# Optimization experiments

Measured on AMD Instinct MI355X. Metric: run time of the kernel, lower is better.

The kernel has to match this reference:

```python
import jax, jax.numpy as jnp
import numpy as np

N = 100000   # nodes
D = 128      # feature dim
E = 1600000  # edges (avg degree 16)
BN_EPS = 1e-5


def setup_inputs() -> dict:
    key = jax.random.key(0)
    ks = jax.random.split(key, 8)
    x = jax.random.normal(ks[0], (N, D), dtype=jnp.float32)
    edge_index = jax.random.randint(ks[1], (2, E), 0, N, dtype=jnp.int64)
    W = jax.random.normal(ks[2], (D, D), dtype=jnp.float32) * 0.05   # GCNConv linear weight
    b = jax.random.normal(ks[3], (D,), dtype=jnp.float32) * 0.05     # GCNConv bias
    gamma = jax.random.uniform(ks[4], (D,), dtype=jnp.float32) + 0.5 # BN weight
    beta = jax.random.normal(ks[5], (D,), dtype=jnp.float32) * 0.1   # BN bias
    running_mean = jax.random.normal(ks[6], (D,), dtype=jnp.float32) * 0.1
    running_var = jax.random.uniform(ks[7], (D,), dtype=jnp.float32) + 0.5
    return {"x": x, "edge_index": edge_index, "W": W, "b": b,
            "gamma": gamma, "beta": beta,
            "running_mean": running_mean, "running_var": running_var}


def reference(x, edge_index, W, b, gamma, beta, running_mean, running_var):
    # --- GCNConv (default: add self-loops, symmetric normalization) ---
    h = x @ W                                        # [N, D]
    loops = jnp.arange(N, dtype=edge_index.dtype)
    src = jnp.concatenate([edge_index[0], loops])    # [E+N]
    dst = jnp.concatenate([edge_index[1], loops])    # [E+N]
    deg = jax.ops.segment_sum(jnp.ones_like(dst, dtype=h.dtype), dst, num_segments=N)
    dinv = jax.lax.rsqrt(jnp.maximum(deg, 1.0))      # deg >= 1 due to self-loops
    norm = dinv[src] * dinv[dst]                     # [E+N]
    agg = jax.ops.segment_sum(h[src] * norm[:, None], dst, num_segments=N)  # [N, D]
    agg = agg + b
    # --- BatchNorm1d (inference: running stats) ---
    bn = (agg - running_mean) * jax.lax.rsqrt(running_var + BN_EPS) * gamma + beta
    # --- ReLU + residual (dropout is identity in eval) ---
    return jax.nn.relu(bn) + x
```

## Files before the change

kernel.cpp:

```cpp
#include <hip/hip_runtime.h>

#define D 128
#define BN_EPS 1e-5f
#define NBUCK 512
#define BSHIFT 8
#define BNODES 256

using short8 = __attribute__((ext_vector_type(8))) short;
using floatx4 = __attribute__((ext_vector_type(4))) float;

__device__ inline unsigned short f2bf(float f) {
    unsigned u = __float_as_uint(f);
    u += 0x7fff + ((u >> 16) & 1);
    return (unsigned short)(u >> 16);
}
__device__ inline float bf2f(unsigned short s) {
    return __uint_as_float(((unsigned)s) << 16);
}

__global__ void wt_kernel(const float* __restrict__ W, const float* __restrict__ b,
                          const float* __restrict__ gamma, const float* __restrict__ beta,
                          const float* __restrict__ mean, const float* __restrict__ var,
                          unsigned short* __restrict__ Wt, float* __restrict__ scv,
                          float* __restrict__ pov) {
    int t = blockIdx.x * blockDim.x + threadIdx.x;
    int k = t >> 7, n = t & 127;
    Wt[(size_t)n * D + k] = f2bf(W[t]);
    if (t < D) {
        float sc = gamma[t] * rsqrtf(var[t] + BN_EPS);
        scv[t] = sc;
        pov[t] = (b[t] - mean[t]) * sc + beta[t];
    }
}

__global__ __launch_bounds__(512) void pAwt_kernel(
    const int* __restrict__ dst, int* __restrict__ bucketTot, int E,
    const float* __restrict__ W, const float* __restrict__ b,
    const float* __restrict__ gamma, const float* __restrict__ beta,
    const float* __restrict__ mean, const float* __restrict__ var,
    unsigned short* __restrict__ Wt, float* __restrict__ scv,
    float* __restrict__ pov) {
    __shared__ int lh[NBUCK];
    int tid = threadIdx.x;
    lh[tid] = 0;
    __syncthreads();
    for (int i = blockIdx.x * 512 + tid; i < E; i += gridDim.x * 512)
        atomicAdd(&lh[dst[i] >> BSHIFT], 1);
    if (blockIdx.x < 16) {
        int t = blockIdx.x * 512 + tid;
#pragma unroll
        for (int h = 0; h < 2; ++h) {
            int tt = t + h * 8192;
            Wt[(size_t)(tt & 127) * D + (tt >> 7)] = f2bf(W[tt]);
        }
        if (blockIdx.x == 0 && tid < D) {
            float sc = gamma[tid] * rsqrtf(var[tid] + BN_EPS);
            scv[tid] = sc;
            pov[tid] = (b[tid] - mean[tid]) * sc + beta[tid];
        }
    }
    __syncthreads();
    if (lh[tid]) atomicAdd(&bucketTot[tid], lh[tid]);
}

__global__ __launch_bounds__(512) void pB_kernel(const int* __restrict__ src,
                                                 const int* __restrict__ dst,
                                                 const int* __restrict__ bucketTot,
                                                 int* __restrict__ resCnt,
                                                 int2* __restrict__ pairs, int E) {
    __shared__ int sb[NBUCK];
    __shared__ int lh[NBUCK];
    __shared__ int lcur[NBUCK];
    int tid = threadIdx.x;
    sb[tid] = bucketTot[tid];
    lh[tid] = 0;
    __syncthreads();
    for (int d = 1; d < NBUCK; d <<= 1) {
        int v = (tid >= d) ? sb[tid - d] : 0;
        __syncthreads();
        sb[tid] += v;
        __syncthreads();
    }
    int chunk = (E + gridDim.x - 1) / gridDim.x;
    int base = blockIdx.x * chunk;
    int lim = min(chunk, E - base);
    if (lim <= 0) return;
    for (int i = tid; i < lim; i += 512) atomicAdd(&lh[dst[base + i] >> BSHIFT], 1);
    __syncthreads();
    int c = lh[tid];
    lcur[tid] = c ? (sb[tid] - bucketTot[tid]) + atomicAdd(&resCnt[tid], c) : 0;
    __syncthreads();
    for (int i = tid; i < lim; i += 512) {
        int s = src[base + i], d2 = dst[base + i];
        int pos = atomicAdd(&lcur[d2 >> BSHIFT], 1);
        pairs[pos] = make_int2(s, d2);
    }
}

__global__ __launch_bounds__(512) void sortxs_kernel(
    const int2* __restrict__ pairs, const int* __restrict__ bucketTot,
    const float* __restrict__ x, int* __restrict__ deg, int* __restrict__ offs,
    int* __restrict__ colidx, float* __restrict__ dinv,
    unsigned short* __restrict__ xs, int N, int E) {
    __shared__ int sb[NBUCK];
    __shared__ int lh[BNODES];
    __shared__ int lcur[BNODES];
    __shared__ float sdv[BNODES];
    int tid = threadIdx.x;
    int b = blockIdx.x;
    sb[tid] = bucketTot[tid];
    __syncthreads();
    for (int d = 1; d < NBUCK; d <<= 1) {
        int v = (tid >= d) ? sb[tid - d] : 0;
        __syncthreads();
        sb[tid] += v;
        __syncthreads();
    }
    int cnt = bucketTot[b];
    int base = sb[b] - cnt;
    if (tid < BNODES) lh[tid] = 0;
    __syncthreads();
    for (int i = tid; i < cnt; i += 512)
        atomicAdd(&lh[pairs[base + i].y & (BNODES - 1)], 1);
    __syncthreads();
    int orig = (tid < BNODES) ? lh[tid] : 0;
    for (int d = 1; d < BNODES; d <<= 1) {
        int v = (tid < BNODES && tid >= d) ? lh[tid - d] : 0;
        __syncthreads();
        if (tid < BNODES) lh[tid] += v;
        __syncthreads();
    }
    if (tid < BNODES) {
        int exc = lh[tid] - orig;
        int node = b * BNODES + tid;
        float dvv = rsqrtf((float)(orig + 1));
        sdv[tid] = dvv;
        if (node < N) {
            deg[node] = orig;
            offs[node] = base + exc;
            dinv[node] = dvv;
        }
        lcur[tid] = exc;
    }
    if (b == 0 && tid == 0) offs[N] = E;
    __syncthreads();
    for (int i = tid; i < cnt; i += 512) {
        int2 p = pairs[base + i];
        int pos = atomicAdd(&lcur[p.y & (BNODES - 1)], 1);
        colidx[base + pos] = p.x;
    }
    int nb = min(BNODES, N - b * BNODES);
    if (nb > 0) {
        const float4* x4 = (const float4*)x;
        ushort4* xs4 = (ushort4*)xs;
        int tot = nb * 32;
        for (int c = tid; c < tot; c += 512) {
            int nl = c >> 5, q = c & 31;
            int node = b * BNODES + nl;
            float dvv = sdv[nl];
            float4 f = x4[(size_t)node * 32 + q];
            ushort4 o;
            o.x = f2bf(dvv * f.x); o.y = f2bf(dvv * f.y);
            o.z = f2bf(dvv * f.z); o.w = f2bf(dvv * f.w);
            xs4[(size_t)node * 32 + q] = o;
        }
    }
}

__global__ void deg_kernel(const int* __restrict__ dst, int* __restrict__ deg, int E) {
    int e = blockIdx.x * blockDim.x + threadIdx.x;
    if (e < E) atomicAdd(&deg[dst[e]], 1);
}

__global__ void dinv_kernel(const int* __restrict__ deg, float* __restrict__ dinv, int N) {
    int v = blockIdx.x * blockDim.x + threadIdx.x;
    if (v < N) dinv[v] = rsqrtf((float)(deg[v] + 1));
}

__global__ __launch_bounds__(256) void scan1_kernel(const int* __restrict__ deg,
                                                    int* __restrict__ bsum, int N) {
    __shared__ int s[256];
    int t = threadIdx.x;
    int v = blockIdx.x * 256 + t;
    s[t] = (v < N) ? deg[v] : 0;
    for (int st = 128; st > 0; st >>= 1) {
        __syncthreads();
        if (t < st) s[t] += s[t + st];
    }
    if (t == 0) bsum[blockIdx.x] = s[0];
}

__global__ __launch_bounds__(512) void scan2_kernel(int* __restrict__ bsum,
                                                    int* __restrict__ offs, int P, int N) {
    __shared__ int a[512];
    int t = threadIdx.x;
    int orig = (t < P) ? bsum[t] : 0;
    a[t] = orig;
    __syncthreads();
    for (int d = 1; d < 512; d <<= 1) {
        int tv = (t >= d) ? a[t - d] : 0;
        __syncthreads();
        a[t] += tv;
        __syncthreads();
    }
    if (t < P) bsum[t] = a[t] - orig;
    if (t == 0) offs[N] = a[511];
}

__global__ __launch_bounds__(256) void scan3_kernel(const int* __restrict__ deg,
                                                    const int* __restrict__ bsum,
                                                    int* __restrict__ offs,
                                                    int* __restrict__ cursor, int N) {
    __shared__ int a[256];
    int t = threadIdx.x;
    int v = blockIdx.x * 256 + t;
    int d = (v < N) ? deg[v] : 0;
    a[t] = d;
    __syncthreads();
    for (int st = 1; st < 256; st <<= 1) {
        int tv = (t >= st) ? a[t - st] : 0;
        __syncthreads();
        a[t] += tv;
        __syncthreads();
    }
    if (v < N) {
        int off = bsum[blockIdx.x] + a[t] - d;
        offs[v] = off;
        cursor[v] = off;
    }
}

__global__ void fill_kernel(const int* __restrict__ src, const int* __restrict__ dst,
                            int* __restrict__ cursor, int* __restrict__ colidx, int E) {
    int e = blockIdx.x * blockDim.x + threadIdx.x;
    if (e < E) {
        int d = dst[e];
        int pos = atomicAdd(&cursor[d], 1);
        colidx[pos] = src[e];
    }
}

__global__ __launch_bounds__(256) void agg_kernel(
    const float* __restrict__ x, const unsigned short* __restrict__ xs,
    const float* __restrict__ dinv, const int* __restrict__ offs,
    const int* __restrict__ colidx, float* __restrict__ outp,
    unsigned int* __restrict__ aggb, int N) {
    int wid = (blockIdx.x * blockDim.x + threadIdx.x) >> 6;
    if (wid >= N) return;
    int lane = threadIdx.x & 63;
    float dv = dinv[wid];
    float a0, a1;
    int p = offs[wid], pe = offs[wid + 1];
    if (xs) {
        const unsigned int* xs32 = (const unsigned int*)xs;
        unsigned int sv = xs32[(size_t)wid * 64 + lane];
        a0 = bf2f((unsigned short)sv);
        a1 = bf2f((unsigned short)(sv >> 16));
        for (; p + 16 <= pe; p += 16) {
            int u[16];
            unsigned int v[16];
#pragma unroll
            for (int j = 0; j < 16; ++j) u[j] = colidx[p + j];
#pragma unroll
            for (int j = 0; j < 16; ++j) v[j] = xs32[(size_t)u[j] * 64 + lane];
#pragma unroll
            for (int j = 0; j < 16; ++j) {
                a0 += bf2f((unsigned short)v[j]);
                a1 += bf2f((unsigned short)(v[j] >> 16));
            }
        }
        for (; p + 4 <= pe; p += 4) {
            int u[4];
            unsigned int v[4];
#pragma unroll
            for (int j = 0; j < 4; ++j) u[j] = colidx[p + j];
#pragma unroll
            for (int j = 0; j < 4; ++j) v[j] = xs32[(size_t)u[j] * 64 + lane];
#pragma unroll
            for (int j = 0; j < 4; ++j) {
                a0 += bf2f((unsigned short)v[j]);
                a1 += bf2f((unsigned short)(v[j] >> 16));
            }
        }
        for (; p < pe; ++p) {
            unsigned int v = xs32[(size_t)colidx[p] * 64 + lane];
            a0 += bf2f((unsigned short)v);
            a1 += bf2f((unsigned short)(v >> 16));
        }
        aggb[(size_t)wid * 64 + lane] =
            (unsigned int)f2bf(dv * a0) | ((unsigned int)f2bf(dv * a1) << 16);
    } else {
        const float2* x2 = (const float2*)x;
        float2 s = x2[(size_t)wid * 64 + lane];
        a0 = dv * s.x;
        a1 = dv * s.y;
        for (; p < pe; ++p) {
            int u = colidx[p];
            float du = dinv[u];
            float2 vv = x2[(size_t)u * 64 + lane];
            a0 += du * vv.x;
            a1 += du * vv.y;
        }
        float2 r;
        r.x = dv * a0;
        r.y = dv * a1;
        ((float2*)outp)[(size_t)wid * 64 + lane] = r;
    }
}

__global__ __launch_bounds__(256) void gemm_kernel(
    float* __restrict__ outp, const float* __restrict__ xg,
    const unsigned short* __restrict__ Wt, const unsigned short* __restrict__ aggb,
    const float* __restrict__ scv, const float* __restrict__ pov, int nTiles) {
    __shared__ uint4 sW4[2048];
    int tid = threadIdx.x;
    const uint4* W4 = (const uint4*)Wt;
#pragma unroll
    for (int i = 0; i < 8; ++i) {
        int q = tid + i * 256;
        int row = q >> 4, c4 = q & 15;
        sW4[row * 16 + (c4 ^ (row & 7))] = W4[q];
    }
    __syncthreads();

    int wid = (blockIdx.x * blockDim.x + tid) >> 6;
    if (wid >= nTiles) return;
    int lane = tid & 63;
    int m = lane & 15, quad = lane >> 4;
    int row0 = wid * 16;

    short8 A[4];
    if (aggb) {
        const unsigned short* arow = aggb + (size_t)(row0 + m) * D;
#pragma unroll
        for (int ks = 0; ks < 4; ++ks)
            A[ks] = *(const short8*)&arow[ks * 32 + quad * 8];
    } else {
        const float* arow = outp + (size_t)(row0 + m) * D;
#pragma unroll
        for (int ks = 0; ks < 4; ++ks) {
            float4 f0 = *(const float4*)(arow + ks * 32 + quad * 8);
            float4 f1 = *(const float4*)(arow + ks * 32 + quad * 8 + 4);
            short8 af;
            af[0] = (short)f2bf(f0.x); af[1] = (short)f2bf(f0.y);
            af[2] = (short)f2bf(f0.z); af[3] = (short)f2bf(f0.w);
            af[4] = (short)f2bf(f1.x); af[5] = (short)f2bf(f1.y);
            af[6] = (short)f2bf(f1.z); af[7] = (short)f2bf(f1.w);
            A[ks] = af;
        }
    }

#pragma unroll
    for (int cg = 0; cg < 8; ++cg) {
        int brow = cg * 16 + m;
        floatx4 acc = {0.f, 0.f, 0.f, 0.f};
#pragma unroll
        for (int ks = 0; ks < 4; ++ks) {
            short8 Bf = *(const short8*)&sW4[brow * 16 + ((ks * 4 + quad) ^ (m & 7))];
            acc = __builtin_amdgcn_mfma_f32_16x16x32_bf16(A[ks], Bf, acc, 0, 0, 0);
        }
        int col = cg * 16 + m;
        float sc = scv[col], po = pov[col];
#pragma unroll
        for (int i = 0; i < 4; ++i) {
            int row = row0 + quad * 4 + i;
            float bn = acc[i] * sc + po;
            size_t idx = (size_t)row * D + col;
            outp[idx] = fmaxf(bn, 0.f) + xg[idx];
        }
    }
}

extern "C" void kernel_launch(void* const* d_in, const int* in_sizes, int n_in,
                              void* d_out, int out_size, void* d_ws, size_t ws_size,
                              hipStream_t stream) {
    const float* x = (const float*)d_in[0];
    const int* edge = (const int*)d_in[1];
    const float* Wm = (const float*)d_in[2];
    const float* b = (const float*)d_in[3];
    const float* gamma = (const float*)d_in[4];
    const float* beta = (const float*)d_in[5];
    const float* mean = (const float*)d_in[6];
    const float* var = (const float*)d_in[7];
    float* out = (float*)d_out;

    int N = in_sizes[0] / D;
    int E = in_sizes[1] / 2;
    const int* src = edge;
    const int* dst = edge + E;
    int P = (N + 255) / 256;

    char* w = (char*)d_ws;
    size_t cur = 0;
    auto take = [&](size_t bytes) -> void* {
        cur = (cur + 15) & ~(size_t)15;
        void* p = w + cur;
        cur += bytes;
        return p;
    };
    int* deg = (int*)take((size_t)N * 4);
    int* bucketTot = (int*)take(NBUCK * 4);
    int* resCnt = (int*)take(NBUCK * 4);
    float* dinv = (float*)take((size_t)N * 4);
    int* offs = (int*)take((size_t)(N + 1) * 4);
    int* cursor = (int*)take((size_t)N * 4);
    int* bsum = (int*)take((size_t)(P + 1) * 4);
    unsigned short* Wt = (unsigned short*)take((size_t)D * D * 2);
    float* scv = (float*)take(D * 4);
    float* pov = (float*)take(D * 4);
    int* colidx = (int*)take((size_t)E * 4);
    cur = (cur + 15) & ~(size_t)15;
    size_t fixedEnd = cur;

    size_t xsBytes = (size_t)N * D * 2;
    size_t zoneBytes = (xsBytes > (size_t)E * 8) ? xsBytes : (size_t)E * 8;
    bool fast = fixedEnd + xsBytes + zoneBytes <= ws_size;

    unsigned short* xs = nullptr;
    int2* pairs = nullptr;
    unsigned int* aggb = nullptr;
    if (fast) {
        xs = (unsigned short*)(w + fixedEnd);
        pairs = (int2*)(w + fixedEnd + xsBytes);
        aggb = (unsigned int*)(w + fixedEnd + xsBytes);
    }

    if (fast) {
        hipMemsetAsync(bucketTot, 0, (size_t)NBUCK * 8, stream);
        pAwt_kernel<<<1024, 512, 0, stream>>>(dst, bucketTot, E, Wm, b, gamma, beta,
                                              mean, var, Wt, scv, pov);
        pB_kernel<<<1024, 512, 0, stream>>>(src, dst, bucketTot, resCnt, pairs, E);
        sortxs_kernel<<<NBUCK, 512, 0, stream>>>(pairs, bucketTot, x, deg, offs, colidx,
                                                 dinv, xs, N, E);
    } else {
        wt_kernel<<<(D * D) / 256, 256, 0, stream>>>(Wm, b, gamma, beta, mean, var, Wt,
                                                     scv, pov);
        hipMemsetAsync(deg, 0, sizeof(int) * N, stream);
        deg_kernel<<<(E + 255) / 256, 256, 0, stream>>>(dst, deg, E);
        dinv_kernel<<<(N + 255) / 256, 256, 0, stream>>>(deg, dinv, N);
        scan1_kernel<<<P, 256, 0, stream>>>(deg, bsum, N);
        scan2_kernel<<<1, 512, 0, stream>>>(bsum, offs, P, N);
        scan3_kernel<<<P, 256, 0, stream>>>(deg, bsum, offs, cursor, N);
        fill_kernel<<<(E + 255) / 256, 256, 0, stream>>>(src, dst, cursor, colidx, E);
    }
    agg_kernel<<<(N * 64 + 255) / 256, 256, 0, stream>>>(x, xs, dinv, offs, colidx, out,
                                                         aggb, N);
    int nTiles = (N + 15) / 16;
    gemm_kernel<<<(nTiles * 64 + 255) / 256, 256, 0, stream>>>(
        out, x, Wt, (const unsigned short*)aggb, scv, pov, nTiles);
}
```

Before: 286.7 us.

## Replace two-pass bucket sort with fixed-capacity buckets and packed edge pairs

Drops the separate bucket-counting pass by giving each destination bucket a fixed capacity slot region, so edge pairs are scattered in one pass with per-bucket atomic reservation. Pairs are packed into 32 bits (low dst byte in the top 8 bits, src in the low 24) to halve scatter and read traffic. Buckets that overflow fall back to a full edge scan in sort and agg, and agg now derives each row's end from degree instead of the next offset. This removes one full read of dst and a kernel launch. It risks very slow fallback paths if a bucket exceeds capacity, and it limits N to 2^24.

```diff
diff --git a/kernel.cpp b/kernel.cpp
--- a/kernel.cpp
+++ b/kernel.cpp
@@ -5,6 +5,7 @@
 #define NBUCK 512
 #define BSHIFT 8
 #define BNODES 256
+#define CAP 4608
 
 using short8 = __attribute__((ext_vector_type(8))) short;
 using floatx4 = __attribute__((ext_vector_type(4))) float;
@@ -16,6 +17,143 @@
 }
 __device__ inline float bf2f(unsigned short s) {
     return __uint_as_float(((unsigned)s) << 16);
+}
+
+__global__ __launch_bounds__(256) void init_kernel(
+    const float* __restrict__ W, const float* __restrict__ b,
+    const float* __restrict__ gamma, const float* __restrict__ beta,
+    const float* __restrict__ mean, const float* __restrict__ var,
+    unsigned short* __restrict__ Wt, float* __restrict__ scv,
+    float* __restrict__ pov, int* __restrict__ resCnt) {
+    int t = blockIdx.x * 256 + threadIdx.x;
+    Wt[(size_t)(t & 127) * D + (t >> 7)] = f2bf(W[t]);
+    if (t < NBUCK) resCnt[t] = 0;
+    if (t < D) {
+        float sc = gamma[t] * rsqrtf(var[t] + BN_EPS);
+        scv[t] = sc;
+        pov[t] = (b[t] - mean[t]) * sc + beta[t];
+    }
+}
+
+__global__ __launch_bounds__(512) void pB_kernel(const int* __restrict__ src,
+                                                 const int* __restrict__ dst,
+                                                 int* __restrict__ resCnt,
+                                                 unsigned int* __restrict__ pairs,
+                                                 int E) {
+    __shared__ int lh[NBUCK];
+    __shared__ int lcur[NBUCK];
+    int tid = threadIdx.x;
+    lh[tid] = 0;
+    __syncthreads();
+    int chunk = (E + gridDim.x - 1) / gridDim.x;
+    int base = blockIdx.x * chunk;
+    int lim = min(chunk, E - base);
+    if (lim <= 0) return;
+    for (int i = tid; i < lim; i += 512) atomicAdd(&lh[dst[base + i] >> BSHIFT], 1);
+    __syncthreads();
+    int c = lh[tid];
+    lcur[tid] = tid * CAP + (c ? atomicAdd(&resCnt[tid], c) : 0);
+    __syncthreads();
+    for (int i = tid; i < lim; i += 512) {
+        int s = src[base + i], d2 = dst[base + i];
+        int b2 = d2 >> BSHIFT;
+        int pos = atomicAdd(&lcur[b2], 1);
+        if (pos < (b2 + 1) * CAP)
+            pairs[pos] = (((unsigned)d2 & 255u) << 24) | (unsigned)s;
+    }
+}
+
+__global__ __launch_bounds__(512) void sortxs_kernel(
+    const unsigned int* __restrict__ pairs, const int* __restrict__ resCnt,
+    const int* __restrict__ src, const int* __restrict__ dst,
+    const float* __restrict__ x, int* __restrict__ deg, int* __restrict__ offs,
+    int* __restrict__ colidx, float* __restrict__ dinv,
+    unsigned short* __restrict__ xs, int N, int E) {
+    __shared__ int sb[NBUCK];
+    __shared__ int lh[BNODES];
+    __shared__ int lcur[BNODES];
+    __shared__ float sdv[BNODES];
+    int tid = threadIdx.x;
+    int b = blockIdx.x;
+    sb[tid] = resCnt[tid];
+    __syncthreads();
+    for (int d = 1; d < NBUCK; d <<= 1) {
+        int v = (tid >= d) ? sb[tid - d] : 0;
+        __syncthreads();
+        sb[tid] += v;
+        __syncthreads();
+    }
+    int cnt = resCnt[b];
+    int cbase = sb[b] - cnt;
+    int pbase = b * CAP;
+    if (tid < BNODES) lh[tid] = 0;
+    __syncthreads();
+
+    if (cnt <= CAP) {
+        for (int i = tid; i < cnt; i += 512)
+            atomicAdd(&lh[pairs[pbase + i] >> 24], 1);
+        __syncthreads();
+        int orig = (tid < BNODES) ? lh[tid] : 0;
+        for (int d = 1; d < BNODES; d <<= 1) {
+            int v = (tid < BNODES && tid >= d) ? lh[tid - d] : 0;
+            __syncthreads();
+            if (tid < BNODES) lh[tid] += v;
+            __syncthreads();
+        }
+        if (tid < BNODES) {
+            int exc = lh[tid] - orig;
+            int node = b * BNODES + tid;
+            float dvv = rsqrtf((float)(orig + 1));
+            sdv[tid] = dvv;
+            if (node < N) {
+                deg[node] = orig;
+                offs[node] = cbase + exc;
+                dinv[node] = dvv;
+            }
+            lcur[tid] = exc;
+        }
+        __syncthreads();
+        for (int i = tid; i < cnt; i += 512) {
+            unsigned int p = pairs[pbase + i];
+            int pos = atomicAdd(&lcur[p >> 24], 1);
+            colidx[cbase + pos] = (int)(p & 0x00FFFFFFu);
+        }
+    } else {
+        for (int i = tid; i < E; i += 512) {
+            int d2 = dst[i];
+            if ((d2 >> BSHIFT) == b) atomicAdd(&lh[d2 & 255], 1);
+        }
+        __syncthreads();
+        if (tid < BNODES) {
+            int orig = lh[tid];
+            int node = b * BNODES + tid;
+            float dvv = rsqrtf((float)(orig + 1));
+            sdv[tid] = dvv;
+            if (node < N) {
+                deg[node] = orig;
+                offs[node] = -1;
+                dinv[node] = dvv;
+            }
+        }
+        __syncthreads();
+    }
+
+    int nb = min(BNODES, N - b * BNODES);
+    if (nb > 0) {
+        const float4* x4 = (const float4*)x;
+        ushort4* xs4 = (ushort4*)xs;
+        int tot = nb * 32;
+        for (int c2 = tid; c2 < tot; c2 += 512) {
+            int nl = c2 >> 5, q = c2 & 31;
+            int node = b * BNODES + nl;
+            float dvv = sdv[nl];
+            float4 f = x4[(size_t)node * 32 + q];
+            ushort4 o;
+            o.x = f2bf(dvv * f.x); o.y = f2bf(dvv * f.y);
+            o.z = f2bf(dvv * f.z); o.w = f2bf(dvv * f.w);
+            xs4[(size_t)node * 32 + q] = o;
+        }
+    }
 }
 
 __global__ void wt_kernel(const float* __restrict__ W, const float* __restrict__ b,
@@ -33,140 +171,6 @@
     }
 }
 
-__global__ __launch_bounds__(512) void pAwt_kernel(
-    const int* __restrict__ dst, int* __restrict__ bucketTot, int E,
-    const float* __restrict__ W, const float* __restrict__ b,
-    const float* __restrict__ gamma, const float* __restrict__ beta,
-    const float* __restrict__ mean, const float* __restrict__ var,
-    unsigned short* __restrict__ Wt, float* __restrict__ scv,
-    float* __restrict__ pov) {
-    __shared__ int lh[NBUCK];
-    int tid = threadIdx.x;
-    lh[tid] = 0;
-    __syncthreads();
-    for (int i = blockIdx.x * 512 + tid; i < E; i += gridDim.x * 512)
-        atomicAdd(&lh[dst[i] >> BSHIFT], 1);
-    if (blockIdx.x < 16) {
-        int t = blockIdx.x * 512 + tid;
-#pragma unroll
-        for (int h = 0; h < 2; ++h) {
-            int tt = t + h * 8192;
-            Wt[(size_t)(tt & 127) * D + (tt >> 7)] = f2bf(W[tt]);
-        }
-        if (blockIdx.x == 0 && tid < D) {
-            float sc = gamma[tid] * rsqrtf(var[tid] + BN_EPS);
-            scv[tid] = sc;
-            pov[tid] = (b[tid] - mean[tid]) * sc + beta[tid];
-        }
-    }
-    __syncthreads();
-    if (lh[tid]) atomicAdd(&bucketTot[tid], lh[tid]);
-}
-
-__global__ __launch_bounds__(512) void pB_kernel(const int* __restrict__ src,
-                                                 const int* __restrict__ dst,
-                                                 const int* __restrict__ bucketTot,
-                                                 int* __restrict__ resCnt,
-                                                 int2* __restrict__ pairs, int E) {
-    __shared__ int sb[NBUCK];
-    __shared__ int lh[NBUCK];
-    __shared__ int lcur[NBUCK];
-    int tid = threadIdx.x;
-    sb[tid] = bucketTot[tid];
-    lh[tid] = 0;
-    __syncthreads();
-    for (int d = 1; d < NBUCK; d <<= 1) {
-        int v = (tid >= d) ? sb[tid - d] : 0;
-        __syncthreads();
-        sb[tid] += v;
-        __syncthreads();
-    }
-    int chunk = (E + gridDim.x - 1) / gridDim.x;
-    int base = blockIdx.x * chunk;
-    int lim = min(chunk, E - base);
-    if (lim <= 0) return;
-    for (int i = tid; i < lim; i += 512) atomicAdd(&lh[dst[base + i] >> BSHIFT], 1);
-    __syncthreads();
-    int c = lh[tid];
-    lcur[tid] = c ? (sb[tid] - bucketTot[tid]) + atomicAdd(&resCnt[tid], c) : 0;
-    __syncthreads();
-    for (int i = tid; i < lim; i += 512) {
-        int s = src[base + i], d2 = dst[base + i];
-        int pos = atomicAdd(&lcur[d2 >> BSHIFT], 1);
-        pairs[pos] = make_int2(s, d2);
-    }
-}
-
-__global__ __launch_bounds__(512) void sortxs_kernel(
-    const int2* __restrict__ pairs, const int* __restrict__ bucketTot,
-    const float* __restrict__ x, int* __restrict__ deg, int* __restrict__ offs,
-    int* __restrict__ colidx, float* __restrict__ dinv,
-    unsigned short* __restrict__ xs, int N, int E) {
-    __shared__ int sb[NBUCK];
-    __shared__ int lh[BNODES];
-    __shared__ int lcur[BNODES];
-    __shared__ float sdv[BNODES];
-    int tid = threadIdx.x;
-    int b = blockIdx.x;
-    sb[tid] = bucketTot[tid];
-    __syncthreads();
-    for (int d = 1; d < NBUCK; d <<= 1) {
-        int v = (tid >= d) ? sb[tid - d] : 0;
-        __syncthreads();
-        sb[tid] += v;
-        __syncthreads();
-    }
-    int cnt = bucketTot[b];
-    int base = sb[b] - cnt;
-    if (tid < BNODES) lh[tid] = 0;
-    __syncthreads();
-    for (int i = tid; i < cnt; i += 512)
-        atomicAdd(&lh[pairs[base + i].y & (BNODES - 1)], 1);
-    __syncthreads();
-    int orig = (tid < BNODES) ? lh[tid] : 0;
-    for (int d = 1; d < BNODES; d <<= 1) {
-        int v = (tid < BNODES && tid >= d) ? lh[tid - d] : 0;
-        __syncthreads();
-        if (tid < BNODES) lh[tid] += v;
-        __syncthreads();
-    }
-    if (tid < BNODES) {
-        int exc = lh[tid] - orig;
-        int node = b * BNODES + tid;
-        float dvv = rsqrtf((float)(orig + 1));
-        sdv[tid] = dvv;
-        if (node < N) {
-            deg[node] = orig;
-            offs[node] = base + exc;
-            dinv[node] = dvv;
-        }
-        lcur[tid] = exc;
-    }
-    if (b == 0 && tid == 0) offs[N] = E;
-    __syncthreads();
-    for (int i = tid; i < cnt; i += 512) {
-        int2 p = pairs[base + i];
-        int pos = atomicAdd(&lcur[p.y & (BNODES - 1)], 1);
-        colidx[base + pos] = p.x;
-    }
-    int nb = min(BNODES, N - b * BNODES);
-    if (nb > 0) {
-        const float4* x4 = (const float4*)x;
-        ushort4* xs4 = (ushort4*)xs;
-        int tot = nb * 32;
-        for (int c = tid; c < tot; c += 512) {
-            int nl = c >> 5, q = c & 31;
-            int node = b * BNODES + nl;
-            float dvv = sdv[nl];
-            float4 f = x4[(size_t)node * 32 + q];
-            ushort4 o;
-            o.x = f2bf(dvv * f.x); o.y = f2bf(dvv * f.y);
-            o.z = f2bf(dvv * f.z); o.w = f2bf(dvv * f.w);
-            xs4[(size_t)node * 32 + q] = o;
-        }
-    }
-}
-
 __global__ void deg_kernel(const int* __restrict__ dst, int* __restrict__ deg, int E) {
     int e = blockIdx.x * blockDim.x + threadIdx.x;
     if (e < E) atomicAdd(&deg[dst[e]], 1);
@@ -243,49 +247,61 @@
 __global__ __launch_bounds__(256) void agg_kernel(
     const float* __restrict__ x, const unsigned short* __restrict__ xs,
     const float* __restrict__ dinv, const int* __restrict__ offs,
-    const int* __restrict__ colidx, float* __restrict__ outp,
-    unsigned int* __restrict__ aggb, int N) {
+    const int* __restrict__ deg, const int* __restrict__ colidx,
+    const int* __restrict__ src, const int* __restrict__ dst,
+    float* __restrict__ outp, unsigned int* __restrict__ aggb, int N, int E) {
     int wid = (blockIdx.x * blockDim.x + threadIdx.x) >> 6;
     if (wid >= N) return;
     int lane = threadIdx.x & 63;
     float dv = dinv[wid];
     float a0, a1;
-    int p = offs[wid], pe = offs[wid + 1];
+    int p = offs[wid];
     if (xs) {
         const unsigned int* xs32 = (const unsigned int*)xs;
         unsigned int sv = xs32[(size_t)wid * 64 + lane];
         a0 = bf2f((unsigned short)sv);
         a1 = bf2f((unsigned short)(sv >> 16));
-        for (; p + 16 <= pe; p += 16) {
-            int u[16];
-            unsigned int v[16];
-#pragma unroll
-            for (int j = 0; j < 16; ++j) u[j] = colidx[p + j];
-#pragma unroll
-            for (int j = 0; j < 16; ++j) v[j] = xs32[(size_t)u[j] * 64 + lane];
-#pragma unroll
-            for (int j = 0; j < 16; ++j) {
-                a0 += bf2f((unsigned short)v[j]);
-                a1 += bf2f((unsigned short)(v[j] >> 16));
-            }
-        }
-        for (; p + 4 <= pe; p += 4) {
-            int u[4];
-            unsigned int v[4];
-#pragma unroll
-            for (int j = 0; j < 4; ++j) u[j] = colidx[p + j];
-#pragma unroll
-            for (int j = 0; j < 4; ++j) v[j] = xs32[(size_t)u[j] * 64 + lane];
-#pragma unroll
-            for (int j = 0; j < 4; ++j) {
-                a0 += bf2f((unsigned short)v[j]);
-                a1 += bf2f((unsigned short)(v[j] >> 16));
-            }
-        }
-        for (; p < pe; ++p) {
-            unsigned int v = xs32[(size_t)colidx[p] * 64 + lane];
-            a0 += bf2f((unsigned short)v);
-            a1 += bf2f((unsigned short)(v >> 16));
+        if (p >= 0) {
+            int pe = p + deg[wid];
+            for (; p + 16 <= pe; p += 16) {
+                int u[16];
+                unsigned int v[16];
+#pragma unroll
+                for (int j = 0; j < 16; ++j) u[j] = colidx[p + j];
+#pragma unroll
+                for (int j = 0; j < 16; ++j) v[j] = xs32[(size_t)u[j] * 64 + lane];
+#pragma unroll
+                for (int j = 0; j < 16; ++j) {
+                    a0 += bf2f((unsigned short)v[j]);
+                    a1 += bf2f((unsigned short)(v[j] >> 16));
+                }
+            }
+            for (; p + 4 <= pe; p += 4) {
+                int u[4];
+                unsigned int v[4];
+#pragma unroll
+                for (int j = 0; j < 4; ++j) u[j] = colidx[p + j];
+#pragma unroll
+                for (int j = 0; j < 4; ++j) v[j] = xs32[(size_t)u[j] * 64 + lane];
+#pragma unroll
+                for (int j = 0; j < 4; ++j) {
+                    a0 += bf2f((unsigned short)v[j]);
+                    a1 += bf2f((unsigned short)(v[j] >> 16));
+                }
+            }
+            for (; p < pe; ++p) {
+                unsigned int v = xs32[(size_t)colidx[p] * 64 + lane];
+                a0 += bf2f((unsigned short)v);
+                a1 += bf2f((unsigned short)(v >> 16));
+            }
+        } else {
+            for (int e = 0; e < E; ++e) {
+                if (dst[e] == wid) {
+                    unsigned int v = xs32[(size_t)src[e] * 64 + lane];
+                    a0 += bf2f((unsigned short)v);
+                    a1 += bf2f((unsigned short)(v >> 16));
+                }
+            }
         }
         aggb[(size_t)wid * 64 + lane] =
             (unsigned int)f2bf(dv * a0) | ((unsigned int)f2bf(dv * a1) << 16);
@@ -294,6 +310,7 @@
         float2 s = x2[(size_t)wid * 64 + lane];
         a0 = dv * s.x;
         a1 = dv * s.y;
+        int pe = p + deg[wid];
         for (; p < pe; ++p) {
             int u = colidx[p];
             float du = dinv[u];
@@ -351,15 +368,15 @@
     }
 
 #pragma unroll
-    for (int cg = 0; cg < 8; ++cg) {
-        int brow = cg * 16 + m;
+    for (int cg2 = 0; cg2 < 8; ++cg2) {
+        int brow = cg2 * 16 + m;
         floatx4 acc = {0.f, 0.f, 0.f, 0.f};
 #pragma unroll
         for (int ks = 0; ks < 4; ++ks) {
             short8 Bf = *(const short8*)&sW4[brow * 16 + ((ks * 4 + quad) ^ (m & 7))];
             acc = __builtin_amdgcn_mfma_f32_16x16x32_bf16(A[ks], Bf, acc, 0, 0, 0);
         }
-        int col = cg * 16 + m;
+        int col = cg2 * 16 + m;
         float sc = scv[col], po = pov[col];
 #pragma unroll
         for (int i = 0; i < 4; ++i) {
@@ -399,7 +416,6 @@
         return p;
     };
     int* deg = (int*)take((size_t)N * 4);
-    int* bucketTot = (int*)take(NBUCK * 4);
     int* resCnt = (int*)take(NBUCK * 4);
     float* dinv = (float*)take((size_t)N * 4);
     int* offs = (int*)take((size_t)(N + 1) * 4);
@@ -413,25 +429,30 @@
     size_t fixedEnd = cur;
 
     size_t xsBytes = (size_t)N * D * 2;
-    size_t zoneBytes = (xsBytes > (size_t)E * 8) ? xsBytes : (size_t)E * 8;
-    bool fast = fixedEnd + xsBytes + zoneBytes <= ws_size;
+    size_t pairsBytes = (size_t)NBUCK * CAP * 4;
+    size_t zoneBytes = (xsBytes > pairsBytes) ? xsBytes : pairsBytes;
+    bool fast = (fixedEnd + xsBytes + zoneBytes <= ws_size) && (N < (1 << 24));
 
     unsigned short* xs = nullptr;
-    int2* pairs = nullptr;
+    unsigned int* pairs = nullptr;
     unsigned int* aggb = nullptr;
     if (fast) {
         xs = (unsigned short*)(w + fixedEnd);
-        pairs = (int2*)(w + fixedEnd + xsBytes);
+        pairs = (unsigned int*)(w + fixedEnd + xsBytes);
         aggb = (unsigned int*)(w + fixedEnd + xsBytes);
     }
 
     if (fast) {
-        hipMemsetAsync(bucketTot, 0, (size_t)NBUCK * 8, stream);
-        pAwt_kernel<<<1024, 512, 0, stream>>>(dst, bucketTot, E, Wm, b, gamma, beta,
-                                              mean, var, Wt, scv, pov);
-        pB_kernel<<<1024, 512, 0, stream>>>(src, dst, bucketTot, resCnt, pairs, E);
-        sortxs_kernel<<<NBUCK, 512, 0, stream>>>(pairs, bucketTot, x, deg, offs, colidx,
-                                                 dinv, xs, N, E);
+        init_kernel<<<(D * D) / 256, 256, 0, stream>>>(Wm, b, gamma, beta, mean, var,
+                                                       Wt, scv, pov, resCnt);
+        pB_kernel<<<128, 512, 0, stream>>>(src, dst, resCnt, pairs, E);
+        sortxs_kernel<<<NBUCK, 512, 0, stream>>>(pairs, resCnt, src, dst, x, deg, offs,
+                                                 colidx, dinv, xs, N, E);
+        agg_kernel<<<(N * 64 + 255) / 256, 256, 0, stream>>>(
+            x, xs, dinv, offs, deg, colidx, src, dst, out, aggb, N, E);
+        int nTiles = (N + 15) / 16;
+        gemm_kernel<<<(nTiles * 64 + 255) / 256, 256, 0, stream>>>(
+            out, x, Wt, (const unsigned short*)aggb, scv, pov, nTiles);
     } else {
         wt_kernel<<<(D * D) / 256, 256, 0, stream>>>(Wm, b, gamma, beta, mean, var, Wt,
                                                      scv, pov);
@@ -442,10 +463,10 @@
         scan2_kernel<<<1, 512, 0, stream>>>(bsum, offs, P, N);
         scan3_kernel<<<P, 256, 0, stream>>>(deg, bsum, offs, cursor, N);
         fill_kernel<<<(E + 255) / 256, 256, 0, stream>>>(src, dst, cursor, colidx, E);
-    }
-    agg_kernel<<<(N * 64 + 255) / 256, 256, 0, stream>>>(x, xs, dinv, offs, colidx, out,
-                                                         aggb, N);
-    int nTiles = (N + 15) / 16;
-    gemm_kernel<<<(nTiles * 64 + 255) / 256, 256, 0, stream>>>(
-        out, x, Wt, (const unsigned short*)aggb, scv, pov, nTiles);
-}
+        agg_kernel<<<(N * 64 + 255) / 256, 256, 0, stream>>>(
+            x, nullptr, dinv, offs, deg, colidx, src, dst, out, nullptr, N, E);
+        int nTiles = (N + 15) / 16;
+        gemm_kernel<<<(nTiles * 64 + 255) / 256, 256, 0, stream>>>(out, x, Wt, nullptr,
+                                                                   scv, pov, nTiles);
+    }
+}
```

New measurement: 263.8 us. -8.0%, faster.
